# Kernel optimization log

Measured on AMD Instinct MI355X. Metric: run time of the kernel, lower is better.

The kernel has to match this reference:

```python
import jax, jax.numpy as jnp
import numpy as np

N = 1024
D = 128          # node_dim
NUM_LAYERS = 3
H_CLS = 128      # edge classifier hidden


def setup_inputs() -> dict:
    key = jax.random.key(0)
    ks = jax.random.split(key, 20)
    s_in = 1.0 / np.sqrt(3.0)
    s_d = 1.0 / np.sqrt(D)
    s_2d = 1.0 / np.sqrt(2 * D)
    s_h = 1.0 / np.sqrt(H_CLS)
    inp = {
        "node_features": jax.random.uniform(ks[0], (N, 3), jnp.float32),
        "adj_matrix": jax.random.uniform(ks[1], (N, N), jnp.float32),
        "edge_weights": jax.random.normal(ks[2], (N, N, 1), jnp.float32),
        # node embedding Linear(3, D)
        "W_embed": jax.random.uniform(ks[3], (3, D), jnp.float32, -s_in, s_in),
        "b_embed": jax.random.uniform(ks[4], (D,), jnp.float32, -s_in, s_in),
        # stacked GCN layer params, [L, ...]
        "Wu": jax.random.uniform(ks[5], (NUM_LAYERS, D, D), jnp.float32, -s_d, s_d),
        "bu": jax.random.uniform(ks[6], (NUM_LAYERS, D), jnp.float32, -s_d, s_d),
        "Wv": jax.random.uniform(ks[7], (NUM_LAYERS, D, D), jnp.float32, -s_d, s_d),
        "bv": jax.random.uniform(ks[8], (NUM_LAYERS, D), jnp.float32, -s_d, s_d),
        "Wg": jax.random.uniform(ks[9], (NUM_LAYERS, 2 * D, D), jnp.float32, -s_2d, s_2d),
        "bg": jax.random.uniform(ks[10], (NUM_LAYERS, D), jnp.float32, -s_2d, s_2d),
        # edge classifier: Linear(2D, 128) -> ReLU -> Linear(128, 1)
        "Wc1": jax.random.uniform(ks[11], (2 * D, H_CLS), jnp.float32, -s_2d, s_2d),
        "bc1": jax.random.uniform(ks[12], (H_CLS,), jnp.float32, -s_2d, s_2d),
        "Wc2": jax.random.uniform(ks[13], (H_CLS, 1), jnp.float32, -s_h, s_h),
        "bc2": jax.random.uniform(ks[14], (1,), jnp.float32, -s_h, s_h),
    }
    return inp


def reference(node_features, adj_matrix, edge_weights,
              W_embed, b_embed, Wu, bu, Wv, bv, Wg, bg,
              Wc1, bc1, Wc2, bc2):
    h = node_features @ W_embed + b_embed                       # [N, D]
    for l in range(NUM_LAYERS):
        u = h @ Wu[l] + bu[l]                                   # [N, D]
        v = h @ Wv[l] + bv[l]                                   # [N, D]
        agg = adj_matrix @ v                                    # [N, D]
        # gate Linear(2D, D) on cat([u, agg]) == u @ Wg[:D] + agg @ Wg[D:]
        gate = jax.nn.sigmoid(u @ Wg[l, :D] + agg @ Wg[l, D:] + bg[l])
        h = jax.nn.relu(h + gate * agg)
    # edge classifier: cat([h_i, h_j]) @ Wc1 == (h @ Wc1[:D])[i] + (h @ Wc1[D:])[j]
    hi = h @ Wc1[:D]                                            # [N, H]
    hj = h @ Wc1[D:]                                            # [N, H]
    hidden = jax.nn.relu(hi[:, None, :] + hj[None, :, :] + bc1) # [N, N, H]
    logits = jnp.einsum('ijh,h->ij', hidden, Wc2[:, 0]) + bc2[0]  # [N, N]
    loss = jnp.mean(jnp.square(logits * adj_matrix - edge_weights[..., 0]))
    return logits, loss
```

## Files before the change

### kernel.cpp

```cpp
#include <hip/hip_runtime.h>

#define NN 1024
#define DD 128
#define NBLK 256

typedef __attribute__((ext_vector_type(4))) float f32x4;

__device__ __forceinline__ void gridbar(unsigned* bar, unsigned ep) {
    __syncthreads();
    if (threadIdx.x == 0) {
        __threadfence();
        unsigned old = __hip_atomic_fetch_add(&bar[(blockIdx.x & 15) << 5], 1u,
                                              __ATOMIC_RELAXED, __HIP_MEMORY_SCOPE_AGENT);
        if (old == (ep << 4) - 1) {
            unsigned mold = __hip_atomic_fetch_add(&bar[512], 1u,
                                                   __ATOMIC_RELAXED, __HIP_MEMORY_SCOPE_AGENT);
            if (mold == (ep << 4) - 1)
                __hip_atomic_store(&bar[544], ep, __ATOMIC_RELAXED, __HIP_MEMORY_SCOPE_AGENT);
        }
        while (__hip_atomic_load(&bar[544], __ATOMIC_RELAXED, __HIP_MEMORY_SCOPE_AGENT) < ep)
            __builtin_amdgcn_s_sleep(4);
        __threadfence();
    }
    __syncthreads();
}

__device__ __forceinline__ float dotW(const float* __restrict__ W, const float* x, int d) {
    float a0 = 0.f, a1 = 0.f, a2 = 0.f, a3 = 0.f;
#pragma unroll 8
    for (int k = 0; k < DD; k += 4) {
        f32x4 x4 = *(const f32x4*)(x + k);
        a0 = fmaf(W[(k + 0) * DD + d], x4[0], a0);
        a1 = fmaf(W[(k + 1) * DD + d], x4[1], a1);
        a2 = fmaf(W[(k + 2) * DD + d], x4[2], a2);
        a3 = fmaf(W[(k + 3) * DD + d], x4[3], a3);
    }
    return (a0 + a1) + (a2 + a3);
}

__global__ __launch_bounds__(1024, 4) void k_fused(
    const float* __restrict__ adj, const float* __restrict__ ew,
    const float* __restrict__ nf, const float* __restrict__ We, const float* __restrict__ be,
    const float* __restrict__ Wu, const float* __restrict__ bu,
    const float* __restrict__ Wv, const float* __restrict__ bv,
    const float* __restrict__ Wg, const float* __restrict__ bg,
    const float* __restrict__ Wc1, const float* __restrict__ bc1,
    const float* __restrict__ Wc2, const float* __restrict__ bc2,
    float* __restrict__ v0, float* __restrict__ v1,
    float* __restrict__ hi, float* __restrict__ hj,
    float* __restrict__ S1, float* __restrict__ S2,
    float* __restrict__ lossAcc, unsigned* __restrict__ counter,
    unsigned* __restrict__ barCnt, float* __restrict__ outL)
{
    __shared__ float hS[4][DD], uS[4][DD], wS[DD];
    __shared__ union {
        struct {
            float adjS[4][NN];
            float pS[8][4][DD];
            float aggS[4][DD];
            float gacc[2][4][DD];
            float sred[2][4][2];
        } g;
        struct {
            float hiS[64][132];
            float hjS[32][134];
            float lred[16];
        } e;
    } sm;

    int tid = threadIdx.x, bx = blockIdx.x;
    int row0 = bx * 4;
    unsigned ep = 0;

    {
        int r = tid >> 8, k0 = (tid & 255) << 2;
        *(f32x4*)&sm.g.adjS[r][k0] = *(const f32x4*)(adj + (size_t)(row0 + r) * NN + k0);
    }
    if (tid < 512) {
        int r = tid >> 7, d = tid & 127;
        float a = be[d];
#pragma unroll
        for (int k = 0; k < 3; ++k) a = fmaf(nf[(row0 + r) * 3 + k], We[k * DD + d], a);
        hS[r][d] = a;
    }
    __syncthreads();
    {
        int half = tid >> 9, r = (tid >> 7) & 3, d = tid & 127;
        float av = dotW(half ? Wv : Wu, hS[r], d);
        if (!half) uS[r][d] = av + bu[d];
        else       v0[(size_t)(row0 + r) * DD + d] = av + bv[d];
    }
    gridbar(barCnt, ++ep);

    for (int l = 0; l < 3; ++l) {
        const float* vin = (l & 1) ? v1 : v0;
        float* vout = (l & 1) ? v0 : v1;

        {
            int kk = tid >> 7, d = tid & 127;
            int kb = kk << 7;
            float ac0 = 0.f, ac1 = 0.f, ac2 = 0.f, ac3 = 0.f;
#pragma unroll 2
            for (int k = 0; k < 128; k += 4) {
                f32x4 a0 = *(const f32x4*)&sm.g.adjS[0][kb + k];
                f32x4 a1 = *(const f32x4*)&sm.g.adjS[1][kb + k];
                f32x4 a2 = *(const f32x4*)&sm.g.adjS[2][kb + k];
                f32x4 a3 = *(const f32x4*)&sm.g.adjS[3][kb + k];
                const float* vp = vin + (size_t)(kb + k) * DD + d;
                float vk0 = vp[0], vk1 = vp[DD], vk2 = vp[2 * DD], vk3 = vp[3 * DD];
                ac0 = fmaf(a0[0], vk0, ac0); ac1 = fmaf(a1[0], vk0, ac1);
                ac2 = fmaf(a2[0], vk0, ac2); ac3 = fmaf(a3[0], vk0, ac3);
                ac0 = fmaf(a0[1], vk1, ac0); ac1 = fmaf(a1[1], vk1, ac1);
                ac2 = fmaf(a2[1], vk1, ac2); ac3 = fmaf(a3[1], vk1, ac3);
                ac0 = fmaf(a0[2], vk2, ac0); ac1 = fmaf(a1[2], vk2, ac1);
                ac2 = fmaf(a2[2], vk2, ac2); ac3 = fmaf(a3[2], vk2, ac3);
                ac0 = fmaf(a0[3], vk3, ac0); ac1 = fmaf(a1[3], vk3, ac1);
                ac2 = fmaf(a2[3], vk3, ac2); ac3 = fmaf(a3[3], vk3, ac3);
            }
            sm.g.pS[kk][0][d] = ac0; sm.g.pS[kk][1][d] = ac1;
            sm.g.pS[kk][2][d] = ac2; sm.g.pS[kk][3][d] = ac3;
        }
        __syncthreads();
        if (tid < 512) {
            int r = tid >> 7, d = tid & 127;
            float s = 0.f;
#pragma unroll
            for (int c = 0; c < 8; ++c) s += sm.g.pS[c][r][d];
            sm.g.aggS[r][d] = s;
        }
        __syncthreads();
        {
            int half = tid >> 9, r = (tid >> 7) & 3, d = tid & 127;
            const float* WA = Wg + l * (2 * DD * DD) + (half ? DD * DD : 0);
            sm.g.gacc[half][r][d] = dotW(WA, half ? sm.g.aggS[r] : uS[r], d);
        }
        __syncthreads();
        if (tid < 512) {
            int r = tid >> 7, d = tid & 127;
            float g = 1.f / (1.f + __expf(-(sm.g.gacc[0][r][d] + sm.g.gacc[1][r][d] + bg[l * DD + d])));
            float nh = fmaf(g, sm.g.aggS[r][d], hS[r][d]);
            hS[r][d] = nh > 0.f ? nh : 0.f;
        }
        __syncthreads();
        {
            int half = tid >> 9, r = (tid >> 7) & 3, d = tid & 127;
            const float* W2 = (l < 2) ? ((half ? Wv : Wu) + (l + 1) * DD * DD)
                                      : (Wc1 + (half ? DD * DD : 0));
            float av = dotW(W2, hS[r], d);
            if (l < 2) {
                if (!half) uS[r][d] = av + bu[(l + 1) * DD + d];
                else       vout[(size_t)(row0 + r) * DD + d] = av + bv[(l + 1) * DD + d];
            } else {
                float val = av + (half ? 0.f : bc1[d]);
                (half ? hj : hi)[(size_t)(row0 + r) * DD + d] = val;
                float p = val * Wc2[d];
#pragma unroll
                for (int off = 32; off; off >>= 1) p += __shfl_down(p, off);
                if ((tid & 63) == 0) sm.g.sred[half][r][(tid >> 6) & 1] = p;
            }
        }
        if (l == 2) {
            __syncthreads();
            if (tid < 4) S1[row0 + tid] = sm.g.sred[0][tid][0] + sm.g.sred[0][tid][1];
            else if (tid < 8) S2[row0 + tid - 4] = sm.g.sred[1][tid - 4][0] + sm.g.sred[1][tid - 4][1];
        }
        gridbar(barCnt, ++ep);
    }

    if (tid < 128) wS[tid] = Wc2[tid];
    float lsum = 0.f;
    float bcv = bc2[0];
    for (int t = bx; t < 512; t += NBLK) {
        int i0 = (t >> 5) << 6;
        int j0 = (t & 31) << 5;
        __syncthreads();
        for (int e2 = tid; e2 < 64 * 128; e2 += 1024) {
            int r = e2 >> 7, hh = e2 & 127;
            sm.e.hiS[r][hh] = hi[(size_t)(i0 + r) * DD + hh];
        }
        for (int e2 = tid; e2 < 32 * 128; e2 += 1024) {
            int r = e2 >> 7, hh = e2 & 127;
            sm.e.hjS[r][hh] = hj[(size_t)(j0 + r) * DD + hh];
        }
        __syncthreads();
        int i = tid >> 4;
        int j2 = (tid & 15) << 1;
        float acc0 = 0.f, acc1 = 0.f;
#pragma unroll 4
        for (int hh = 0; hh < 128; hh += 4) {
            f32x4 a4 = *(const f32x4*)&sm.e.hiS[i][hh];
            f32x4 b0 = *(const f32x4*)&sm.e.hjS[j2][hh];
            f32x4 b1 = *(const f32x4*)&sm.e.hjS[j2 + 1][hh];
            f32x4 w4 = *(const f32x4*)&wS[hh];
#pragma unroll
            for (int q = 0; q < 4; ++q) {
                acc0 = fmaf(fabsf(a4[q] + b0[q]), w4[q], acc0);
                acc1 = fmaf(fabsf(a4[q] + b1[q]), w4[q], acc1);
            }
        }
        float s1 = S1[i0 + i];
        float2 s2 = *(const float2*)(S2 + j0 + j2);
        float lg0 = fmaf(0.5f, acc0 + s1 + s2.x, bcv);
        float lg1 = fmaf(0.5f, acc1 + s1 + s2.y, bcv);
        size_t off = (size_t)(i0 + i) * NN + j0 + j2;
        float2 lg; lg.x = lg0; lg.y = lg1;
        *(float2*)(outL + off) = lg;
        float2 a2 = *(const float2*)(adj + off);
        float2 e2v = *(const float2*)(ew + off);
        float t0 = fmaf(lg0, a2.x, -e2v.x);
        float t1 = fmaf(lg1, a2.y, -e2v.y);
        lsum = fmaf(t0, t0, fmaf(t1, t1, lsum));
    }
#pragma unroll
    for (int off = 32; off; off >>= 1) lsum += __shfl_down(lsum, off);
    if ((tid & 63) == 0) sm.e.lred[tid >> 6] = lsum;
    __syncthreads();
    if (tid == 0) {
        float bls = 0.f;
#pragma unroll
        for (int w = 0; w < 16; ++w) bls += sm.e.lred[w];
        atomicAdd(lossAcc, bls);
        __threadfence();
        unsigned old = atomicAdd(counter, 1u);
        if (old == NBLK - 1u) {
            __threadfence();
            outL[(size_t)NN * NN] = (*(volatile float*)lossAcc) * (1.f / (1024.f * 1024.f));
        }
    }
}

extern "C" void kernel_launch(void* const* d_in, const int* in_sizes, int n_in,
                              void* d_out, int out_size, void* d_ws, size_t ws_size,
                              hipStream_t stream)
{
    const float* nf  = (const float*)d_in[0];
    const float* adj = (const float*)d_in[1];
    const float* ew  = (const float*)d_in[2];
    const float* We  = (const float*)d_in[3];
    const float* be  = (const float*)d_in[4];
    const float* Wu  = (const float*)d_in[5];
    const float* bu  = (const float*)d_in[6];
    const float* Wv  = (const float*)d_in[7];
    const float* bv  = (const float*)d_in[8];
    const float* Wg  = (const float*)d_in[9];
    const float* bg  = (const float*)d_in[10];
    const float* Wc1 = (const float*)d_in[11];
    const float* bc1 = (const float*)d_in[12];
    const float* Wc2 = (const float*)d_in[13];
    const float* bc2 = (const float*)d_in[14];

    float* ws = (float*)d_ws;
    float* v0  = ws;
    float* v1  = ws + 131072;
    float* hi  = ws + 262144;
    float* hj  = ws + 393216;
    float* S1  = ws + 524288;
    float* S2  = ws + 525312;
    float* lossAcc = ws + 526336;
    unsigned* counter = (unsigned*)(ws + 526337);
    unsigned* barCnt = (unsigned*)(ws + 526368);

    hipMemsetAsync((void*)lossAcc, 0, 2560, stream);
    k_fused<<<NBLK, 1024, 0, stream>>>(adj, ew, nf, We, be, Wu, bu, Wv, bv, Wg, bg,
                                       Wc1, bc1, Wc2, bc2, v0, v1, hi, hj, S1, S2,
                                       lossAcc, counter, barCnt, (float*)d_out);
}
```

Measured before the change: 215.4 us.

## Transpose node-state layouts, register-block small GEMMs, and retile edge classifier

Node states and the adjacency rows are now kept transposed in shared memory, so each weight element loaded from global memory is reused across all four rows. The dense layer matvecs now run on 256 threads instead of 1024. The adj@v aggregation splits into 32 k-chunks with float4 vector loads of v, and the partial sums are reduced in shared memory. The edge classifier changes from two 64x32 tiles per block to a single 64x64 tile per block with 2x2 register blocking, which cuts shared-memory loads per output. The trade-off is less thread parallelism in the matvec phases and a longer 32-way reduction.

```diff
diff --git a/kernel.cpp b/kernel.cpp
--- a/kernel.cpp
+++ b/kernel.cpp
@@ -23,19 +23,6 @@
         __threadfence();
     }
     __syncthreads();
-}
-
-__device__ __forceinline__ float dotW(const float* __restrict__ W, const float* x, int d) {
-    float a0 = 0.f, a1 = 0.f, a2 = 0.f, a3 = 0.f;
-#pragma unroll 8
-    for (int k = 0; k < DD; k += 4) {
-        f32x4 x4 = *(const f32x4*)(x + k);
-        a0 = fmaf(W[(k + 0) * DD + d], x4[0], a0);
-        a1 = fmaf(W[(k + 1) * DD + d], x4[1], a1);
-        a2 = fmaf(W[(k + 2) * DD + d], x4[2], a2);
-        a3 = fmaf(W[(k + 3) * DD + d], x4[3], a3);
-    }
-    return (a0 + a1) + (a2 + a3);
 }
 
 __global__ __launch_bounds__(1024, 4) void k_fused(
@@ -52,20 +39,13 @@
     float* __restrict__ lossAcc, unsigned* __restrict__ counter,
     unsigned* __restrict__ barCnt, float* __restrict__ outL)
 {
-    __shared__ float hS[4][DD], uS[4][DD], wS[DD];
+    __shared__ float hT[DD][4], uT[DD][4], aggT[DD][4];
+    __shared__ float gg[2][4][DD];
+    __shared__ float sred[2][4][2];
+    __shared__ float wS[DD];
     __shared__ union {
-        struct {
-            float adjS[4][NN];
-            float pS[8][4][DD];
-            float aggS[4][DD];
-            float gacc[2][4][DD];
-            float sred[2][4][2];
-        } g;
-        struct {
-            float hiS[64][132];
-            float hjS[32][134];
-            float lred[16];
-        } e;
+        struct { float adjT[NN][4]; float pS[32][4][DD]; } g;
+        struct { float hiS[64][132]; float hjS[64][132]; float lred[16]; } e;
     } sm;
 
     int tid = threadIdx.x, bx = blockIdx.x;
@@ -74,157 +54,208 @@
 
     {
         int r = tid >> 8, k0 = (tid & 255) << 2;
-        *(f32x4*)&sm.g.adjS[r][k0] = *(const f32x4*)(adj + (size_t)(row0 + r) * NN + k0);
+        f32x4 a = *(const f32x4*)(adj + (size_t)(row0 + r) * NN + k0);
+#pragma unroll
+        for (int i = 0; i < 4; ++i) sm.g.adjT[k0 + i][r] = a[i];
     }
     if (tid < 512) {
         int r = tid >> 7, d = tid & 127;
         float a = be[d];
 #pragma unroll
         for (int k = 0; k < 3; ++k) a = fmaf(nf[(row0 + r) * 3 + k], We[k * DD + d], a);
-        hS[r][d] = a;
+        hT[d][r] = a;
     }
     __syncthreads();
-    {
-        int half = tid >> 9, r = (tid >> 7) & 3, d = tid & 127;
-        float av = dotW(half ? Wv : Wu, hS[r], d);
-        if (!half) uS[r][d] = av + bu[d];
-        else       v0[(size_t)(row0 + r) * DD + d] = av + bv[d];
+    if (tid < 256) {
+        int half = tid >> 7, d = tid & 127;
+        const float* W = half ? Wv : Wu;
+        float acc[4] = {0.f, 0.f, 0.f, 0.f};
+#pragma unroll 8
+        for (int k = 0; k < DD; ++k) {
+            f32x4 x4 = *(const f32x4*)&hT[k][0];
+            float w = W[k * DD + d];
+#pragma unroll
+            for (int r = 0; r < 4; ++r) acc[r] = fmaf(x4[r], w, acc[r]);
+        }
+        if (!half) {
+            float bb = bu[d];
+#pragma unroll
+            for (int r = 0; r < 4; ++r) uT[d][r] = acc[r] + bb;
+        } else {
+            float bb = bv[d];
+#pragma unroll
+            for (int r = 0; r < 4; ++r) v0[(size_t)(row0 + r) * DD + d] = acc[r] + bb;
+        }
     }
     gridbar(barCnt, ++ep);
 
     for (int l = 0; l < 3; ++l) {
-        const float* vin = (l & 1) ? v1 : v0;
-        float* vout = (l & 1) ? v0 : v1;
+        const float* vin = (l == 1) ? v1 : v0;
+        float* vout = (l == 0) ? v1 : v0;
 
         {
-            int kk = tid >> 7, d = tid & 127;
-            int kb = kk << 7;
-            float ac0 = 0.f, ac1 = 0.f, ac2 = 0.f, ac3 = 0.f;
-#pragma unroll 2
-            for (int k = 0; k < 128; k += 4) {
-                f32x4 a0 = *(const f32x4*)&sm.g.adjS[0][kb + k];
-                f32x4 a1 = *(const f32x4*)&sm.g.adjS[1][kb + k];
-                f32x4 a2 = *(const f32x4*)&sm.g.adjS[2][kb + k];
-                f32x4 a3 = *(const f32x4*)&sm.g.adjS[3][kb + k];
-                const float* vp = vin + (size_t)(kb + k) * DD + d;
-                float vk0 = vp[0], vk1 = vp[DD], vk2 = vp[2 * DD], vk3 = vp[3 * DD];
-                ac0 = fmaf(a0[0], vk0, ac0); ac1 = fmaf(a1[0], vk0, ac1);
-                ac2 = fmaf(a2[0], vk0, ac2); ac3 = fmaf(a3[0], vk0, ac3);
-                ac0 = fmaf(a0[1], vk1, ac0); ac1 = fmaf(a1[1], vk1, ac1);
-                ac2 = fmaf(a2[1], vk1, ac2); ac3 = fmaf(a3[1], vk1, ac3);
-                ac0 = fmaf(a0[2], vk2, ac0); ac1 = fmaf(a1[2], vk2, ac1);
-                ac2 = fmaf(a2[2], vk2, ac2); ac3 = fmaf(a3[2], vk2, ac3);
-                ac0 = fmaf(a0[3], vk3, ac0); ac1 = fmaf(a1[3], vk3, ac1);
-                ac2 = fmaf(a2[3], vk3, ac2); ac3 = fmaf(a3[3], vk3, ac3);
-            }
-            sm.g.pS[kk][0][d] = ac0; sm.g.pS[kk][1][d] = ac1;
-            sm.g.pS[kk][2][d] = ac2; sm.g.pS[kk][3][d] = ac3;
+            int kk = tid >> 5, dq = tid & 31;
+            int d0 = dq << 2, kb = kk << 5;
+            f32x4 ac0 = {0.f,0.f,0.f,0.f}, ac1 = ac0, ac2 = ac0, ac3 = ac0;
+#pragma unroll 4
+            for (int k = kb; k < kb + 32; ++k) {
+                f32x4 a4 = *(const f32x4*)&sm.g.adjT[k][0];
+                f32x4 v4 = *(const f32x4*)(vin + (size_t)k * DD + d0);
+#pragma unroll
+                for (int c = 0; c < 4; ++c) {
+                    ac0[c] = fmaf(a4[0], v4[c], ac0[c]);
+                    ac1[c] = fmaf(a4[1], v4[c], ac1[c]);
+                    ac2[c] = fmaf(a4[2], v4[c], ac2[c]);
+                    ac3[c] = fmaf(a4[3], v4[c], ac3[c]);
+                }
+            }
+            *(f32x4*)&sm.g.pS[kk][0][d0] = ac0;
+            *(f32x4*)&sm.g.pS[kk][1][d0] = ac1;
+            *(f32x4*)&sm.g.pS[kk][2][d0] = ac2;
+            *(f32x4*)&sm.g.pS[kk][3][d0] = ac3;
         }
         __syncthreads();
         if (tid < 512) {
             int r = tid >> 7, d = tid & 127;
             float s = 0.f;
 #pragma unroll
-            for (int c = 0; c < 8; ++c) s += sm.g.pS[c][r][d];
-            sm.g.aggS[r][d] = s;
-        }
-        __syncthreads();
-        {
-            int half = tid >> 9, r = (tid >> 7) & 3, d = tid & 127;
-            const float* WA = Wg + l * (2 * DD * DD) + (half ? DD * DD : 0);
-            sm.g.gacc[half][r][d] = dotW(WA, half ? sm.g.aggS[r] : uS[r], d);
+            for (int c = 0; c < 32; ++c) s += sm.g.pS[c][r][d];
+            aggT[d][r] = s;
+        }
+        __syncthreads();
+        if (tid < 256) {
+            int half = tid >> 7, d = tid & 127;
+            const float* W = Wg + l * (2 * DD * DD) + (half ? DD * DD : 0);
+            const float (*xT)[4] = half ? aggT : uT;
+            float acc[4] = {0.f, 0.f, 0.f, 0.f};
+#pragma unroll 8
+            for (int k = 0; k < DD; ++k) {
+                f32x4 x4 = *(const f32x4*)&xT[k][0];
+                float w = W[k * DD + d];
+#pragma unroll
+                for (int r = 0; r < 4; ++r) acc[r] = fmaf(x4[r], w, acc[r]);
+            }
+#pragma unroll
+            for (int r = 0; r < 4; ++r) gg[half][r][d] = acc[r];
         }
         __syncthreads();
         if (tid < 512) {
             int r = tid >> 7, d = tid & 127;
-            float g = 1.f / (1.f + __expf(-(sm.g.gacc[0][r][d] + sm.g.gacc[1][r][d] + bg[l * DD + d])));
-            float nh = fmaf(g, sm.g.aggS[r][d], hS[r][d]);
-            hS[r][d] = nh > 0.f ? nh : 0.f;
-        }
-        __syncthreads();
-        {
-            int half = tid >> 9, r = (tid >> 7) & 3, d = tid & 127;
+            float g = 1.f / (1.f + __expf(-(gg[0][r][d] + gg[1][r][d] + bg[l * DD + d])));
+            float nh = fmaf(g, aggT[d][r], hT[d][r]);
+            hT[d][r] = nh > 0.f ? nh : 0.f;
+        }
+        __syncthreads();
+        if (tid < 256) {
+            int half = tid >> 7, d = tid & 127;
             const float* W2 = (l < 2) ? ((half ? Wv : Wu) + (l + 1) * DD * DD)
                                       : (Wc1 + (half ? DD * DD : 0));
-            float av = dotW(W2, hS[r], d);
+            float acc[4] = {0.f, 0.f, 0.f, 0.f};
+#pragma unroll 8
+            for (int k = 0; k < DD; ++k) {
+                f32x4 x4 = *(const f32x4*)&hT[k][0];
+                float w = W2[k * DD + d];
+#pragma unroll
+                for (int r = 0; r < 4; ++r) acc[r] = fmaf(x4[r], w, acc[r]);
+            }
             if (l < 2) {
-                if (!half) uS[r][d] = av + bu[(l + 1) * DD + d];
-                else       vout[(size_t)(row0 + r) * DD + d] = av + bv[(l + 1) * DD + d];
+                if (!half) {
+                    float bb = bu[(l + 1) * DD + d];
+#pragma unroll
+                    for (int r = 0; r < 4; ++r) uT[d][r] = acc[r] + bb;
+                } else {
+                    float bb = bv[(l + 1) * DD + d];
+#pragma unroll
+                    for (int r = 0; r < 4; ++r) vout[(size_t)(row0 + r) * DD + d] = acc[r] + bb;
+                }
             } else {
-                float val = av + (half ? 0.f : bc1[d]);
-                (half ? hj : hi)[(size_t)(row0 + r) * DD + d] = val;
-                float p = val * Wc2[d];
-#pragma unroll
-                for (int off = 32; off; off >>= 1) p += __shfl_down(p, off);
-                if ((tid & 63) == 0) sm.g.sred[half][r][(tid >> 6) & 1] = p;
+                float bcv = half ? 0.f : bc1[d];
+                float* out2 = half ? hj : hi;
+                float wv = Wc2[d];
+                int w2 = (tid >> 6) & 1;
+#pragma unroll
+                for (int r = 0; r < 4; ++r) {
+                    float val = acc[r] + bcv;
+                    out2[(size_t)(row0 + r) * DD + d] = val;
+                    float p = val * wv;
+#pragma unroll
+                    for (int off = 32; off; off >>= 1) p += __shfl_down(p, off);
+                    if ((tid & 63) == 0) sred[half][r][w2] = p;
+                }
             }
         }
         if (l == 2) {
             __syncthreads();
-            if (tid < 4) S1[row0 + tid] = sm.g.sred[0][tid][0] + sm.g.sred[0][tid][1];
-            else if (tid < 8) S2[row0 + tid - 4] = sm.g.sred[1][tid - 4][0] + sm.g.sred[1][tid - 4][1];
+            if (tid < 4) S1[row0 + tid] = sred[0][tid][0] + sred[0][tid][1];
+            else if (tid < 8) S2[row0 + tid - 4] = sred[1][tid - 4][0] + sred[1][tid - 4][1];
         }
         gridbar(barCnt, ++ep);
     }
 
-    if (tid < 128) wS[tid] = Wc2[tid];
-    float lsum = 0.f;
-    float bcv = bc2[0];
-    for (int t = bx; t < 512; t += NBLK) {
-        int i0 = (t >> 5) << 6;
-        int j0 = (t & 31) << 5;
-        __syncthreads();
-        for (int e2 = tid; e2 < 64 * 128; e2 += 1024) {
-            int r = e2 >> 7, hh = e2 & 127;
-            sm.e.hiS[r][hh] = hi[(size_t)(i0 + r) * DD + hh];
-        }
-        for (int e2 = tid; e2 < 32 * 128; e2 += 1024) {
-            int r = e2 >> 7, hh = e2 & 127;
-            sm.e.hjS[r][hh] = hj[(size_t)(j0 + r) * DD + hh];
-        }
-        __syncthreads();
-        int i = tid >> 4;
-        int j2 = (tid & 15) << 1;
-        float acc0 = 0.f, acc1 = 0.f;
+    {
+        int i0 = (bx >> 4) << 6, j0 = (bx & 15) << 6;
+        if (tid < 128) wS[tid] = Wc2[tid];
+        for (int e2 = tid; e2 < 2048; e2 += 1024) {
+            int r = e2 >> 5, c = (e2 & 31) << 2;
+            *(f32x4*)&sm.e.hiS[r][c] = *(const f32x4*)(hi + (size_t)(i0 + r) * DD + c);
+            *(f32x4*)&sm.e.hjS[r][c] = *(const f32x4*)(hj + (size_t)(j0 + r) * DD + c);
+        }
+        __syncthreads();
+        int ty = tid >> 5, tx = tid & 31;
+        int ia = ty << 1, ja = tx << 1;
+        float a00 = 0.f, a01 = 0.f, a10 = 0.f, a11 = 0.f;
 #pragma unroll 4
-        for (int hh = 0; hh < 128; hh += 4) {
-            f32x4 a4 = *(const f32x4*)&sm.e.hiS[i][hh];
-            f32x4 b0 = *(const f32x4*)&sm.e.hjS[j2][hh];
-            f32x4 b1 = *(const f32x4*)&sm.e.hjS[j2 + 1][hh];
+        for (int hh = 0; hh < DD; hh += 4) {
+            f32x4 x0 = *(const f32x4*)&sm.e.hiS[ia][hh];
+            f32x4 x1 = *(const f32x4*)&sm.e.hiS[ia + 1][hh];
+            f32x4 y0 = *(const f32x4*)&sm.e.hjS[ja][hh];
+            f32x4 y1 = *(const f32x4*)&sm.e.hjS[ja + 1][hh];
             f32x4 w4 = *(const f32x4*)&wS[hh];
 #pragma unroll
             for (int q = 0; q < 4; ++q) {
-                acc0 = fmaf(fabsf(a4[q] + b0[q]), w4[q], acc0);
-                acc1 = fmaf(fabsf(a4[q] + b1[q]), w4[q], acc1);
-            }
-        }
-        float s1 = S1[i0 + i];
-        float2 s2 = *(const float2*)(S2 + j0 + j2);
-        float lg0 = fmaf(0.5f, acc0 + s1 + s2.x, bcv);
-        float lg1 = fmaf(0.5f, acc1 + s1 + s2.y, bcv);
-        size_t off = (size_t)(i0 + i) * NN + j0 + j2;
-        float2 lg; lg.x = lg0; lg.y = lg1;
-        *(float2*)(outL + off) = lg;
-        float2 a2 = *(const float2*)(adj + off);
-        float2 e2v = *(const float2*)(ew + off);
-        float t0 = fmaf(lg0, a2.x, -e2v.x);
-        float t1 = fmaf(lg1, a2.y, -e2v.y);
-        lsum = fmaf(t0, t0, fmaf(t1, t1, lsum));
-    }
-#pragma unroll
-    for (int off = 32; off; off >>= 1) lsum += __shfl_down(lsum, off);
-    if ((tid & 63) == 0) sm.e.lred[tid >> 6] = lsum;
-    __syncthreads();
-    if (tid == 0) {
-        float bls = 0.f;
-#pragma unroll
-        for (int w = 0; w < 16; ++w) bls += sm.e.lred[w];
-        atomicAdd(lossAcc, bls);
-        __threadfence();
-        unsigned old = atomicAdd(counter, 1u);
-        if (old == NBLK - 1u) {
+                a00 = fmaf(fabsf(x0[q] + y0[q]), w4[q], a00);
+                a01 = fmaf(fabsf(x0[q] + y1[q]), w4[q], a01);
+                a10 = fmaf(fabsf(x1[q] + y0[q]), w4[q], a10);
+                a11 = fmaf(fabsf(x1[q] + y1[q]), w4[q], a11);
+            }
+        }
+        float bcv = bc2[0];
+        int i = i0 + ia, j = j0 + ja;
+        float s1a = S1[i], s1b = S1[i + 1];
+        float2 s2 = *(const float2*)(S2 + j);
+        float lg00 = fmaf(0.5f, a00 + s1a + s2.x, bcv);
+        float lg01 = fmaf(0.5f, a01 + s1a + s2.y, bcv);
+        float lg10 = fmaf(0.5f, a10 + s1b + s2.x, bcv);
+        float lg11 = fmaf(0.5f, a11 + s1b + s2.y, bcv);
+        size_t o0 = (size_t)i * NN + j, o1 = o0 + NN;
+        float2 w0; w0.x = lg00; w0.y = lg01;
+        float2 w1; w1.x = lg10; w1.y = lg11;
+        *(float2*)(outL + o0) = w0;
+        *(float2*)(outL + o1) = w1;
+        float2 aa0 = *(const float2*)(adj + o0);
+        float2 aa1 = *(const float2*)(adj + o1);
+        float2 ee0 = *(const float2*)(ew + o0);
+        float2 ee1 = *(const float2*)(ew + o1);
+        float t0 = fmaf(lg00, aa0.x, -ee0.x);
+        float t1 = fmaf(lg01, aa0.y, -ee0.y);
+        float t2 = fmaf(lg10, aa1.x, -ee1.x);
+        float t3 = fmaf(lg11, aa1.y, -ee1.y);
+        float ls = fmaf(t0, t0, fmaf(t1, t1, fmaf(t2, t2, t3 * t3)));
+#pragma unroll
+        for (int off = 32; off; off >>= 1) ls += __shfl_down(ls, off);
+        if ((tid & 63) == 0) sm.e.lred[tid >> 6] = ls;
+        __syncthreads();
+        if (tid == 0) {
+            float bls = 0.f;
+#pragma unroll
+            for (int w = 0; w < 16; ++w) bls += sm.e.lred[w];
+            atomicAdd(lossAcc, bls);
             __threadfence();
-            outL[(size_t)NN * NN] = (*(volatile float*)lossAcc) * (1.f / (1024.f * 1024.f));
+            unsigned old = atomicAdd(counter, 1u);
+            if (old == NBLK - 1u) {
+                __threadfence();
+                outL[(size_t)NN * NN] = (*(volatile float*)lossAcc) * (1.f / (1024.f * 1024.f));
+            }
         }
     }
 }
```

Measured after the change: 223.8 us. 3.9% more time.
